# Kernel tuning notes

Measured on AMD Instinct MI355X. Metric: run time of the kernel, lower is better.

The kernel has to match this reference:

```python
import jax, jax.numpy as jnp
import numpy as np

L = 5        # num_layers
D = 128      # emb_dim
H = 2 * D    # mlp hidden
N_ATOM_FEATS, ATOM_VOCAB = 9, 120
N_BOND_FEATS, BOND_VOCAB = 3, 6
BN_EPS = 1e-5


def setup_inputs() -> dict:
    key = jax.random.key(0)
    ks = jax.random.split(key, 16)
    N, E = 200000, 400000
    x = jax.random.randint(ks[0], (N, N_ATOM_FEATS), 0, ATOM_VOCAB)
    edge_index = jax.random.randint(ks[1], (2, E), 0, N)
    edge_attr = jax.random.randint(ks[2], (E, N_BOND_FEATS), 0, BOND_VOCAB)
    s = 0.02
    return {
        "x": x,
        "edge_index": edge_index,
        "edge_attr": edge_attr,
        "atom_emb": jax.random.normal(ks[3], (N_ATOM_FEATS, ATOM_VOCAB, D), jnp.float32) * s,
        "bond_emb": jax.random.normal(ks[4], (L, N_BOND_FEATS, BOND_VOCAB, D), jnp.float32) * s,
        "W1": jax.random.normal(ks[5], (L, D, H), jnp.float32) * s,
        "b1": jnp.zeros((L, H), jnp.float32),
        "bn1_g": jnp.ones((L, H), jnp.float32),
        "bn1_b": jnp.zeros((L, H), jnp.float32),
        "W2": jax.random.normal(ks[6], (L, H, D), jnp.float32) * s,
        "b2": jnp.zeros((L, D), jnp.float32),
        "eps": jnp.zeros((L,), jnp.float32),
        "out_bn_g": jnp.ones((L, D), jnp.float32),
        "out_bn_b": jnp.zeros((L, D), jnp.float32),
    }


def _batchnorm(z, g, b):
    mu = jnp.mean(z, axis=0, keepdims=True)
    var = jnp.var(z, axis=0, keepdims=True)
    return (z - mu) * jax.lax.rsqrt(var + BN_EPS) * g + b


def _multi_embed(tables, idx):
    # tables: [F, V, D], idx: [N, F] -> sum_f tables[f][idx[:, f]] : [N, D]
    gathered = jax.vmap(lambda tab, i: tab[i], in_axes=(0, 1))(tables, idx)  # [F, N, D]
    return jnp.sum(gathered, axis=0)


def reference(x, edge_index, edge_attr, atom_emb, bond_emb, W1, b1, bn1_g, bn1_b,
              W2, b2, eps, out_bn_g, out_bn_b):
    N = x.shape[0]
    src, dst = edge_index[0], edge_index[1]
    h = _multi_embed(atom_emb, x)  # AtomEncoder: [N, D]
    for l in range(L):
        e = _multi_embed(bond_emb[l], edge_attr)          # BondEncoder: [E, D]
        msg = jax.nn.relu(h[src] + e)                     # message
        aggr = jax.ops.segment_sum(msg, dst, num_segments=N)  # scatter-add
        z = (1.0 + eps[l]) * h + aggr                     # GIN combine
        z = jax.nn.relu(_batchnorm(z @ W1[l] + b1[l], bn1_g[l], bn1_b[l]))
        z = z @ W2[l] + b2[l]
        h = jax.nn.relu(_batchnorm(z, out_bn_g[l], out_bn_b[l]))  # relu+dropout(p=0)
    return h  # JK='last'
```

## Files before the change

### kernel.cpp

```cpp
#include <hip/hip_runtime.h>

#define NF_ATOM 9
#define NF_BOND 3
#define DD 128
#define HH 256
#define NLAYER 5
#define NSHARD 32
#define NCODE 216

typedef float fv4 __attribute__((ext_vector_type(4)));
typedef __bf16 bfv8 __attribute__((ext_vector_type(8)));
typedef unsigned int uv4 __attribute__((ext_vector_type(4)));

__device__ inline unsigned short f2bf(float f) {
    unsigned int u = __builtin_bit_cast(unsigned int, f);
    u = u + 0x7FFFu + ((u >> 16) & 1u);
    return (unsigned short)(u >> 16);
}
__device__ inline float bf2f(unsigned short s) {
    unsigned int u = ((unsigned int)s) << 16;
    return __builtin_bit_cast(float, u);
}

__global__ __launch_bounds__(256) void k_atom(const int* __restrict__ x,
        const float* __restrict__ emb, unsigned short* __restrict__ h, int N) {
    int gid = blockIdx.x * 256 + threadIdx.x;
    int n = gid >> 5;
    if (n >= N) return;
    int c = (gid & 31) << 2;
    const int* xr = x + n * NF_ATOM;
    float4 acc = make_float4(0.f, 0.f, 0.f, 0.f);
#pragma unroll
    for (int f = 0; f < NF_ATOM; ++f) {
        int idx = xr[f];
        float4 v = *(const float4*)(emb + ((size_t)(f * 120 + idx) * DD) + c);
        acc.x += v.x; acc.y += v.y; acc.z += v.z; acc.w += v.w;
    }
    ushort4 o;
    o.x = f2bf(acc.x); o.y = f2bf(acc.y); o.z = f2bf(acc.z); o.w = f2bf(acc.w);
    *(ushort4*)(h + (size_t)n * DD + c) = o;
}

__global__ __launch_bounds__(256) void k_wconv(const float* __restrict__ W1,
        const float* __restrict__ W2, unsigned short* __restrict__ W1t,
        unsigned short* __restrict__ W2t) {
    int id = blockIdx.x * 256 + threadIdx.x;
    const int T1 = NLAYER * 4 * 256 * 32;
    if (id < T1) {
        int k = id & 31, n = (id >> 5) & 255, kc = (id >> 13) & 3, l = id >> 15;
        W1t[id] = f2bf(W1[((size_t)(l * 128 + kc * 32 + k)) * 256 + n]);
    } else {
        int id2 = id - T1;
        if (id2 >= NLAYER * 8 * 128 * 32) return;
        int k = id2 & 31, n = (id2 >> 5) & 127, kc = (id2 >> 12) & 7, l = id2 >> 15;
        W2t[id2] = f2bf(W2[((size_t)(l * 256 + kc * 32 + k)) * 128 + n]);
    }
}

__global__ __launch_bounds__(256) void k_bsumtab(const float* __restrict__ bemb,
        float* __restrict__ tab) {
    int id = blockIdx.x * 256 + threadIdx.x;
    if (id >= NLAYER * NCODE * DD) return;
    int c = id & 127;
    int code = (id >> 7) % NCODE;
    int l = id / (NCODE * DD);
    int a0 = code % 6, a1 = (code / 6) % 6, a2 = code / 36;
    const float* bl = bemb + (size_t)l * NF_BOND * 6 * DD;
    tab[id] = bl[(0 * 6 + a0) * DD + c] + bl[(1 * 6 + a1) * DD + c] + bl[(2 * 6 + a2) * DD + c];
}

__global__ __launch_bounds__(256) void k_deg(const int* __restrict__ ei, int* __restrict__ deg, int E) {
    int e = blockIdx.x * 256 + threadIdx.x;
    if (e < E) atomicAdd(&deg[ei[E + e]], 1);
}
__global__ __launch_bounds__(256) void k_bsum(const int* __restrict__ deg, int* __restrict__ bsum, int N) {
    __shared__ int red[256];
    int t = threadIdx.x, b = blockIdx.x;
    int i0 = b * 1024 + t * 4;
    int s = 0;
#pragma unroll
    for (int j = 0; j < 4; ++j) if (i0 + j < N) s += deg[i0 + j];
    red[t] = s; __syncthreads();
    for (int off = 128; off > 0; off >>= 1) {
        if (t < off) red[t] += red[t + off];
        __syncthreads();
    }
    if (t == 0) bsum[b] = red[0];
}
__global__ __launch_bounds__(256) void k_bscan(const int* __restrict__ bsum, int* __restrict__ boff, int nb) {
    __shared__ int ts[256];
    int t = threadIdx.x;
    int v = (t < nb) ? bsum[t] : 0;
    ts[t] = v; __syncthreads();
    for (int off = 1; off < 256; off <<= 1) {
        int u = (t >= off) ? ts[t - off] : 0;
        __syncthreads();
        ts[t] += u;
        __syncthreads();
    }
    if (t < nb) boff[t] = ts[t] - v;
}
__global__ __launch_bounds__(256) void k_csr(const int* deg, const int* __restrict__ boff,
        int* rs, int N, int E) {
    __shared__ int ts[256];
    int t = threadIdx.x, b = blockIdx.x;
    int i0 = b * 1024 + t * 4;
    int d[4];
#pragma unroll
    for (int j = 0; j < 4; ++j) d[j] = (i0 + j < N) ? deg[i0 + j] : 0;
    int tsum = d[0] + d[1] + d[2] + d[3];
    ts[t] = tsum; __syncthreads();
    for (int off = 1; off < 256; off <<= 1) {
        int u = (t >= off) ? ts[t - off] : 0;
        __syncthreads();
        ts[t] += u;
        __syncthreads();
    }
    int base = boff[b] + ts[t] - tsum;
    int p = 0;
#pragma unroll
    for (int j = 0; j < 4; ++j) {
        int dj = d[j];
        if (i0 + j < N) rs[i0 + j] = base + p;
        p += dj;
    }
    if (b == 0 && t == 0) rs[N] = E;
}
__global__ __launch_bounds__(256) void k_scatter(const int* __restrict__ ei,
        const int* __restrict__ ea, int* __restrict__ rs, int* __restrict__ epack, int E) {
    int e = blockIdx.x * 256 + threadIdx.x;
    if (e < E) {
        int pos = atomicAdd(&rs[ei[E + e]], 1);
        int code = ea[e * 3 + 0] + 6 * ea[e * 3 + 1] + 36 * ea[e * 3 + 2];
        epack[pos] = ei[e] | (code << 18);
    }
}

__global__ void k_red(const float* __restrict__ sh, int C, const float* __restrict__ bng,
        const float* __restrict__ bnb, const float* __restrict__ gbias, int useb,
        float invN, float* __restrict__ sc_out, float* __restrict__ sh_out) {
    int t = threadIdx.x;
    if (t >= C) return;
    float a = 0.f, qq = 0.f;
#pragma unroll
    for (int s = 0; s < NSHARD; ++s) {
        a += sh[s * 2 * C + t];
        qq += sh[s * 2 * C + C + t];
    }
    float mu = a * invN;
    float var = qq * invN - mu * mu;
    float r = rsqrtf(var + 1e-5f);
    float sc = bng[t] * r;
    float shift = bnb[t] - mu * sc;
    if (useb) shift += gbias[t] * sc;
    sc_out[t] = sc; sh_out[t] = shift;
}

__device__ inline void edge_acc(ushort4 hv, float4 bv, float4 sc, float4 sh, int mode, float* ag) {
    float h0 = bf2f(hv.x), h1 = bf2f(hv.y), h2 = bf2f(hv.z), h3 = bf2f(hv.w);
    if (mode) {
        h0 = fmaxf(h0 * sc.x + sh.x, 0.f); h1 = fmaxf(h1 * sc.y + sh.y, 0.f);
        h2 = fmaxf(h2 * sc.z + sh.z, 0.f); h3 = fmaxf(h3 * sc.w + sh.w, 0.f);
    }
    ag[0] += fmaxf(h0 + bv.x, 0.f); ag[1] += fmaxf(h1 + bv.y, 0.f);
    ag[2] += fmaxf(h2 + bv.z, 0.f); ag[3] += fmaxf(h3 + bv.w, 0.f);
}

__global__ __launch_bounds__(256) void k_zbuild(const unsigned short* __restrict__ y2h,
        const int* __restrict__ rs, const int* __restrict__ epack,
        const float* __restrict__ btab, const float* __restrict__ sctab,
        const float* __restrict__ shtab, const float* __restrict__ epsv,
        int l, int mode, unsigned short* __restrict__ z, int N) {
    int gid = blockIdx.x * 256 + threadIdx.x;
    int n = gid >> 5;
    if (n >= N) return;
    int c = (gid & 31) << 2;
    float4 sc4 = make_float4(1.f, 1.f, 1.f, 1.f), sh4 = make_float4(0.f, 0.f, 0.f, 0.f);
    if (mode) { sc4 = *(const float4*)(sctab + c); sh4 = *(const float4*)(shtab + c); }
    int p0 = (n == 0) ? 0 : rs[n - 1];
    int p1 = rs[n];
    float ag[4] = {0.f, 0.f, 0.f, 0.f};
    int p = p0;
    for (; p + 2 <= p1; p += 2) {
        int rec0 = epack[p], rec1 = epack[p + 1];
        int s0 = rec0 & 0x3FFFF, s1 = rec1 & 0x3FFFF;
        int c0 = ((unsigned int)rec0) >> 18, c1 = ((unsigned int)rec1) >> 18;
        ushort4 h0 = *(const ushort4*)(y2h + (size_t)s0 * DD + c);
        ushort4 h1 = *(const ushort4*)(y2h + (size_t)s1 * DD + c);
        float4 b0 = *(const float4*)(btab + (size_t)c0 * DD + c);
        float4 b1 = *(const float4*)(btab + (size_t)c1 * DD + c);
        edge_acc(h0, b0, sc4, sh4, mode, ag);
        edge_acc(h1, b1, sc4, sh4, mode, ag);
    }
    if (p < p1) {
        int rec = epack[p];
        int s0 = rec & 0x3FFFF;
        int c0 = ((unsigned int)rec) >> 18;
        ushort4 h0 = *(const ushort4*)(y2h + (size_t)s0 * DD + c);
        float4 b0 = *(const float4*)(btab + (size_t)c0 * DD + c);
        edge_acc(h0, b0, sc4, sh4, mode, ag);
    }
    float ep = 1.0f + epsv[l];
    ushort4 sv = *(const ushort4*)(y2h + (size_t)n * DD + c);
    float hz[4] = {bf2f(sv.x), bf2f(sv.y), bf2f(sv.z), bf2f(sv.w)};
    if (mode) {
        hz[0] = fmaxf(hz[0] * sc4.x + sh4.x, 0.f);
        hz[1] = fmaxf(hz[1] * sc4.y + sh4.y, 0.f);
        hz[2] = fmaxf(hz[2] * sc4.z + sh4.z, 0.f);
        hz[3] = fmaxf(hz[3] * sc4.w + sh4.w, 0.f);
    }
    ushort4 o;
    o.x = f2bf(ep * hz[0] + ag[0]);
    o.y = f2bf(ep * hz[1] + ag[1]);
    o.z = f2bf(ep * hz[2] + ag[2]);
    o.w = f2bf(ep * hz[3] + ag[3]);
    *(ushort4*)(z + (size_t)n * DD + c) = o;
}

__global__ __launch_bounds__(256) void k_stat1(const unsigned short* __restrict__ z,
        const unsigned short* __restrict__ W1l, const float* __restrict__ bias,
        float* __restrict__ shard, int N) {
    __shared__ uv4 zt[64 * 16];
    __shared__ uv4 wt[256 * 4];
    int tid = threadIdx.x;
    int row0 = blockIdx.x * 64;
    int wave = tid >> 6, lane = tid & 63, lq = lane >> 4, lr = lane & 15;
    int rbase = tid >> 4, gz = tid & 15;

    uv4 zr[4];
#pragma unroll
    for (int i = 0; i < 4; ++i)
        zr[i] = *(const uv4*)(z + (size_t)(row0 + i * 16 + rbase) * DD + gz * 8);
    const uv4* wsrc = (const uv4*)W1l;
    uv4 wr[4];
#pragma unroll
    for (int i = 0; i < 4; ++i) wr[i] = wsrc[i * 256 + tid];
#pragma unroll
    for (int i = 0; i < 4; ++i) {
        int row = i * 16 + rbase;
        zt[row * 16 + (gz ^ (row & 15))] = zr[i];
    }

    fv4 acc[4][4];
#pragma unroll
    for (int m = 0; m < 4; ++m)
#pragma unroll
        for (int nb = 0; nb < 4; ++nb) acc[m][nb] = (fv4){0.f, 0.f, 0.f, 0.f};

    for (int kc = 0; kc < 4; ++kc) {
        __syncthreads();
#pragma unroll
        for (int i = 0; i < 4; ++i) {
            int g = i * 256 + tid;
            int wn = g >> 2, gw = g & 3;
            wt[wn * 4 + (gw ^ ((wn >> 1) & 3))] = wr[i];
        }
        __syncthreads();
        if (kc < 3) {
#pragma unroll
            for (int i = 0; i < 4; ++i) wr[i] = wsrc[(size_t)(kc + 1) * 1024 + i * 256 + tid];
        }
        bfv8 a[4], b[4];
#pragma unroll
        for (int m = 0; m < 4; ++m) {
            int row = m * 16 + lr;
            a[m] = __builtin_bit_cast(bfv8, zt[row * 16 + ((kc * 4 + lq) ^ (row & 15))]);
        }
#pragma unroll
        for (int nb = 0; nb < 4; ++nb) {
            int col = wave * 64 + nb * 16 + lr;
            b[nb] = __builtin_bit_cast(bfv8, wt[col * 4 + (lq ^ ((col >> 1) & 3))]);
        }
#pragma unroll
        for (int m = 0; m < 4; ++m)
#pragma unroll
            for (int nb = 0; nb < 4; ++nb)
                acc[m][nb] = __builtin_amdgcn_mfma_f32_16x16x32_bf16(a[m], b[nb], acc[m][nb], 0, 0, 0);
    }

    float bv[4], s[4], q[4];
#pragma unroll
    for (int nb = 0; nb < 4; ++nb) {
        bv[nb] = bias[wave * 64 + nb * 16 + lr];
        s[nb] = 0.f; q[nb] = 0.f;
    }
#pragma unroll
    for (int m = 0; m < 4; ++m)
#pragma unroll
        for (int nb = 0; nb < 4; ++nb)
#pragma unroll
            for (int r = 0; r < 4; ++r) {
                float v = acc[m][nb][r] + bv[nb];
                s[nb] += v; q[nb] += v * v;
            }
#pragma unroll
    for (int nb = 0; nb < 4; ++nb) {
        s[nb] += __shfl_xor(s[nb], 16); s[nb] += __shfl_xor(s[nb], 32);
        q[nb] += __shfl_xor(q[nb], 16); q[nb] += __shfl_xor(q[nb], 32);
    }
    if (lane < 16) {
        int shb = (blockIdx.x & (NSHARD - 1)) * 512;
#pragma unroll
        for (int nb = 0; nb < 4; ++nb) {
            int col = wave * 64 + nb * 16 + lr;
            atomicAdd(shard + shb + col, s[nb]);
            atomicAdd(shard + shb + 256 + col, q[nb]);
        }
    }
}

__global__ __launch_bounds__(256) void k_fgemm(const unsigned short* __restrict__ z,
        const unsigned short* __restrict__ W1l, const unsigned short* __restrict__ W2l,
        const float* __restrict__ sc1, const float* __restrict__ sh1,
        const float* __restrict__ bias2,
        unsigned short* __restrict__ y2h, float* __restrict__ shard, int N) {
    __shared__ uv4 smem[2560];
    uv4* zt = smem;
    uv4* wt = smem + 1024;
    uv4* at = smem;
    uv4* wt2 = smem + 2048;
    int tid = threadIdx.x;
    int row0 = blockIdx.x * 64;
    int wave = tid >> 6, lane = tid & 63, lq = lane >> 4, lr = lane & 15;
    int rbase = tid >> 4, gz = tid & 15;

    uv4 zr[4];
#pragma unroll
    for (int i = 0; i < 4; ++i)
        zr[i] = *(const uv4*)(z + (size_t)(row0 + i * 16 + rbase) * DD + gz * 8);
    const uv4* w1src = (const uv4*)W1l;
    uv4 wr[4];
#pragma unroll
    for (int i = 0; i < 4; ++i) wr[i] = w1src[i * 256 + tid];
#pragma unroll
    for (int i = 0; i < 4; ++i) {
        int row = i * 16 + rbase;
        zt[row * 16 + (gz ^ (row & 15))] = zr[i];
    }

    fv4 acc1[4][4];
#pragma unroll
    for (int mc = 0; mc < 4; ++mc)
#pragma unroll
        for (int nr = 0; nr < 4; ++nr) acc1[mc][nr] = (fv4){0.f, 0.f, 0.f, 0.f};

    for (int kc = 0; kc < 4; ++kc) {
        __syncthreads();
#pragma unroll
        for (int i = 0; i < 4; ++i) {
            int g = i * 256 + tid;
            int wn = g >> 2, gw = g & 3;
            wt[wn * 4 + (gw ^ ((wn >> 1) & 3))] = wr[i];
        }
        __syncthreads();
        if (kc < 3) {
#pragma unroll
            for (int i = 0; i < 4; ++i) wr[i] = w1src[(size_t)(kc + 1) * 1024 + i * 256 + tid];
        }
        bfv8 wf[4], zf[4];
#pragma unroll
        for (int mc = 0; mc < 4; ++mc) {
            int col = wave * 64 + mc * 16 + lr;
            wf[mc] = __builtin_bit_cast(bfv8, wt[col * 4 + (lq ^ ((col >> 1) & 3))]);
        }
#pragma unroll
        for (int nr = 0; nr < 4; ++nr) {
            int row = nr * 16 + lr;
            zf[nr] = __builtin_bit_cast(bfv8, zt[row * 16 + ((kc * 4 + lq) ^ (row & 15))]);
        }
#pragma unroll
        for (int mc = 0; mc < 4; ++mc)
#pragma unroll
            for (int nr = 0; nr < 4; ++nr)
                acc1[mc][nr] = __builtin_amdgcn_mfma_f32_16x16x32_bf16(wf[mc], zf[nr], acc1[mc][nr], 0, 0, 0);
    }
    __syncthreads();

    const uv4* w2src = (const uv4*)W2l;
    uv4 wr2[2];
    wr2[0] = w2src[tid]; wr2[1] = w2src[256 + tid];

#pragma unroll
    for (int mc = 0; mc < 4; ++mc) {
        int ycol0 = wave * 64 + mc * 16 + lq * 4;
        float4 s4 = *(const float4*)(sc1 + ycol0);
        float4 h4 = *(const float4*)(sh1 + ycol0);
        int gg = wave * 8 + mc * 2 + (lq >> 1);
#pragma unroll
        for (int nr = 0; nr < 4; ++nr) {
            int zrow = nr * 16 + lr;
            float v0 = fmaxf(acc1[mc][nr][0] * s4.x + h4.x, 0.f);
            float v1 = fmaxf(acc1[mc][nr][1] * s4.y + h4.y, 0.f);
            float v2 = fmaxf(acc1[mc][nr][2] * s4.z + h4.z, 0.f);
            float v3 = fmaxf(acc1[mc][nr][3] * s4.w + h4.w, 0.f);
            uint2 pk;
            pk.x = (unsigned int)f2bf(v0) | ((unsigned int)f2bf(v1) << 16);
            pk.y = (unsigned int)f2bf(v2) | ((unsigned int)f2bf(v3) << 16);
            int gs = gg ^ (zrow & 15);
            ((uint2*)at)[(zrow * 32 + gs) * 2 + (lq & 1)] = pk;
        }
    }

    fv4 acc2[4][2];
#pragma unroll
    for (int m = 0; m < 4; ++m) { acc2[m][0] = (fv4){0.f,0.f,0.f,0.f}; acc2[m][1] = (fv4){0.f,0.f,0.f,0.f}; }

    for (int kc = 0; kc < 8; ++kc) {
        __syncthreads();
        {
            int wn = tid >> 2, gw = tid & 3;
            wt2[wn * 4 + (gw ^ ((wn >> 1) & 3))] = wr2[0];
            int g3 = 256 + tid, wn3 = g3 >> 2, gw3 = g3 & 3;
            wt2[wn3 * 4 + (gw3 ^ ((wn3 >> 1) & 3))] = wr2[1];
        }
        __syncthreads();
        if (kc < 7) {
            wr2[0] = w2src[(size_t)(kc + 1) * 512 + tid];
            wr2[1] = w2src[(size_t)(kc + 1) * 512 + 256 + tid];
        }
        bfv8 a[4], b[2];
#pragma unroll
        for (int m = 0; m < 4; ++m) {
            int row = m * 16 + lr;
            a[m] = __builtin_bit_cast(bfv8, at[row * 32 + ((kc * 4 + lq) ^ (row & 15))]);
        }
#pragma unroll
        for (int nb = 0; nb < 2; ++nb) {
            int col = wave * 32 + nb * 16 + lr;
            b[nb] = __builtin_bit_cast(bfv8, wt2[col * 4 + (lq ^ ((col >> 1) & 3))]);
        }
#pragma unroll
        for (int m = 0; m < 4; ++m)
#pragma unroll
            for (int nb = 0; nb < 2; ++nb)
                acc2[m][nb] = __builtin_amdgcn_mfma_f32_16x16x32_bf16(a[m], b[nb], acc2[m][nb], 0, 0, 0);
    }

    float bv[2], s[2], q[2];
#pragma unroll
    for (int nb = 0; nb < 2; ++nb) {
        bv[nb] = bias2[wave * 32 + nb * 16 + lr];
        s[nb] = 0.f; q[nb] = 0.f;
    }
#pragma unroll
    for (int m = 0; m < 4; ++m)
#pragma unroll
        for (int nb = 0; nb < 2; ++nb) {
            int col = wave * 32 + nb * 16 + lr;
#pragma unroll
            for (int r = 0; r < 4; ++r) {
                float v = acc2[m][nb][r] + bv[nb];
                unsigned short ub = f2bf(v);
                float vr = bf2f(ub);
                int row = row0 + m * 16 + lq * 4 + r;
                y2h[(size_t)row * DD + col] = ub;
                s[nb] += vr; q[nb] += vr * vr;
            }
        }
#pragma unroll
    for (int nb = 0; nb < 2; ++nb) {
        s[nb] += __shfl_xor(s[nb], 16); s[nb] += __shfl_xor(s[nb], 32);
        q[nb] += __shfl_xor(q[nb], 16); q[nb] += __shfl_xor(q[nb], 32);
    }
    if (lane < 16) {
        int shb = (blockIdx.x & (NSHARD - 1)) * 256;
#pragma unroll
        for (int nb = 0; nb < 2; ++nb) {
            int col = wave * 32 + nb * 16 + lr;
            atomicAdd(shard + shb + col, s[nb]);
            atomicAdd(shard + shb + 128 + col, q[nb]);
        }
    }
}

__global__ __launch_bounds__(256) void k_bnfinal(const unsigned short* __restrict__ y2h,
        const float* __restrict__ sc2, const float* __restrict__ sh2,
        float* __restrict__ out, int N) {
    size_t base = ((size_t)blockIdx.x * 256 + threadIdx.x) * 4;
    if (base >= (size_t)N * DD) return;
    int c = (int)(base & (DD - 1));
    ushort4 v = *(const ushort4*)(y2h + base);
    float4 s = *(const float4*)(sc2 + c);
    float4 t = *(const float4*)(sh2 + c);
    float4 o;
    o.x = fmaxf(bf2f(v.x) * s.x + t.x, 0.f);
    o.y = fmaxf(bf2f(v.y) * s.y + t.y, 0.f);
    o.z = fmaxf(bf2f(v.z) * s.z + t.z, 0.f);
    o.w = fmaxf(bf2f(v.w) * s.w + t.w, 0.f);
    *(float4*)(out + base) = o;
}

extern "C" void kernel_launch(void* const* d_in, const int* in_sizes, int n_in,
                              void* d_out, int out_size, void* d_ws, size_t ws_size,
                              hipStream_t stream) {
    const int* x = (const int*)d_in[0];
    const int* ei = (const int*)d_in[1];
    const int* ea = (const int*)d_in[2];
    const float* atom_emb = (const float*)d_in[3];
    const float* bond_emb = (const float*)d_in[4];
    const float* W1 = (const float*)d_in[5];
    const float* b1 = (const float*)d_in[6];
    const float* bn1_g = (const float*)d_in[7];
    const float* bn1_b = (const float*)d_in[8];
    const float* W2 = (const float*)d_in[9];
    const float* b2 = (const float*)d_in[10];
    const float* epsv = (const float*)d_in[11];
    const float* obn_g = (const float*)d_in[12];
    const float* obn_b = (const float*)d_in[13];
    int N = in_sizes[0] / NF_ATOM;
    int E = in_sizes[1] / 2;

    char* wsb = (char*)d_ws;
    unsigned short* y2h = (unsigned short*)wsb;
    unsigned short* zb = (unsigned short*)(wsb + (size_t)N * 256);
    int* epack = (int*)(wsb + (size_t)N * 512);
    unsigned short* w1t = (unsigned short*)(wsb + (size_t)N * 512 + (size_t)E * 4);
    unsigned short* w2t = w1t + 163840;
    float* btab = (float*)((char*)w2t + 327680);
    float* sc1 = btab + NLAYER * NCODE * DD;
    float* sh1 = sc1 + 256;
    float* sc2 = sh1 + 256;
    float* sh2 = sc2 + 128;
    float* shard1 = sh2 + 128;
    float* shard2 = shard1 + NSHARD * 512;
    int* rsarr = (int*)(shard2 + NSHARD * 256);
    int* bsum = rsarr + (N + 1);
    int* boff = bsum + 256;
    float invN = 1.0f / (float)N;
    int nbk = (N + 1023) / 1024;

    k_wconv<<<1280, 256, 0, stream>>>(W1, W2, w1t, w2t);
    k_bsumtab<<<(NLAYER * NCODE * DD + 255) / 256, 256, 0, stream>>>(bond_emb, btab);
    hipMemsetAsync(rsarr, 0, ((size_t)N + 1) * 4, stream);
    k_deg<<<(E + 255) / 256, 256, 0, stream>>>(ei, rsarr, E);
    k_bsum<<<nbk, 256, 0, stream>>>(rsarr, bsum, N);
    k_bscan<<<1, 256, 0, stream>>>(bsum, boff, nbk);
    k_csr<<<nbk, 256, 0, stream>>>(rsarr, boff, rsarr, N, E);
    k_scatter<<<(E + 255) / 256, 256, 0, stream>>>(ei, ea, rsarr, epack, E);
    k_atom<<<(N * 32 + 255) / 256, 256, 0, stream>>>(x, atom_emb, y2h, N);

    int gb = N / 64;
    for (int l = 0; l < NLAYER; ++l) {
        hipMemsetAsync(shard1, 0, (size_t)NSHARD * 768 * sizeof(float), stream);
        k_zbuild<<<(N * 32 + 255) / 256, 256, 0, stream>>>(y2h, rsarr, epack,
                btab + (size_t)l * NCODE * DD, sc2, sh2, epsv, l, (l == 0) ? 0 : 1, zb, N);
        k_stat1<<<gb, 256, 0, stream>>>(zb, w1t + (size_t)l * 32768, b1 + l * HH, shard1, N);
        k_red<<<1, 256, 0, stream>>>(shard1, 256, bn1_g + l * HH, bn1_b + l * HH,
                b1 + l * HH, 1, invN, sc1, sh1);
        k_fgemm<<<gb, 256, 0, stream>>>(zb, w1t + (size_t)l * 32768, w2t + (size_t)l * 32768,
                sc1, sh1, b2 + l * DD, y2h, shard2, N);
        k_red<<<1, 128, 0, stream>>>(shard2, 128, obn_g + l * DD, obn_b + l * DD,
                (const float*)nullptr, 0, invN, sc2, sh2);
    }
    k_bnfinal<<<(int)(((size_t)N * DD / 4 + 255) / 256), 256, 0, stream>>>(
            y2h, sc2, sh2, (float*)d_out, N);
}
```

Baseline: 791.3 us.

## Split bf16 weights into hi/lo parts for higher-precision GEMMs, hoist shard zeroing

Each weight is stored as a bf16 high part plus a bf16 residual. Every GEMM K-loop is doubled so activations multiply both parts and recover near-fp32 weight precision. The per-layer memset of the statistics shards is replaced by one upfront memset over per-layer shard buffers. This is mainly an accuracy fix that doubles MFMA work and weight traffic in the stat and fused GEMM kernels; the memset hoist only saves a few launches.

Result: slower. 1.007 ms (+27.3%).

```diff
diff --git a/kernel.cpp b/kernel.cpp
--- a/kernel.cpp
+++ b/kernel.cpp
@@ -48,12 +48,20 @@
     const int T1 = NLAYER * 4 * 256 * 32;
     if (id < T1) {
         int k = id & 31, n = (id >> 5) & 255, kc = (id >> 13) & 3, l = id >> 15;
-        W1t[id] = f2bf(W1[((size_t)(l * 128 + kc * 32 + k)) * 256 + n]);
+        int o = id & 32767;
+        float w = W1[((size_t)(l * 128 + kc * 32 + k)) * 256 + n];
+        unsigned short hi = f2bf(w);
+        W1t[(size_t)l * 65536 + o] = hi;
+        W1t[(size_t)l * 65536 + 32768 + o] = f2bf(w - bf2f(hi));
     } else {
         int id2 = id - T1;
         if (id2 >= NLAYER * 8 * 128 * 32) return;
         int k = id2 & 31, n = (id2 >> 5) & 127, kc = (id2 >> 12) & 7, l = id2 >> 15;
-        W2t[id2] = f2bf(W2[((size_t)(l * 256 + kc * 32 + k)) * 128 + n]);
+        int o = id2 & 32767;
+        float w = W2[((size_t)(l * 256 + kc * 32 + k)) * 128 + n];
+        unsigned short hi = f2bf(w);
+        W2t[(size_t)l * 65536 + o] = hi;
+        W2t[(size_t)l * 65536 + 32768 + o] = f2bf(w - bf2f(hi));
     }
 }
 
@@ -247,7 +255,7 @@
 #pragma unroll
         for (int nb = 0; nb < 4; ++nb) acc[m][nb] = (fv4){0.f, 0.f, 0.f, 0.f};
 
-    for (int kc = 0; kc < 4; ++kc) {
+    for (int kc = 0; kc < 8; ++kc) {
         __syncthreads();
 #pragma unroll
         for (int i = 0; i < 4; ++i) {
@@ -256,7 +264,7 @@
             wt[wn * 4 + (gw ^ ((wn >> 1) & 3))] = wr[i];
         }
         __syncthreads();
-        if (kc < 3) {
+        if (kc < 7) {
 #pragma unroll
             for (int i = 0; i < 4; ++i) wr[i] = wsrc[(size_t)(kc + 1) * 1024 + i * 256 + tid];
         }
@@ -264,7 +272,7 @@
 #pragma unroll
         for (int m = 0; m < 4; ++m) {
             int row = m * 16 + lr;
-            a[m] = __builtin_bit_cast(bfv8, zt[row * 16 + ((kc * 4 + lq) ^ (row & 15))]);
+            a[m] = __builtin_bit_cast(bfv8, zt[row * 16 + (((kc & 3) * 4 + lq) ^ (row & 15))]);
         }
 #pragma unroll
         for (int nb = 0; nb < 4; ++nb) {
@@ -344,7 +352,7 @@
 #pragma unroll
         for (int nr = 0; nr < 4; ++nr) acc1[mc][nr] = (fv4){0.f, 0.f, 0.f, 0.f};
 
-    for (int kc = 0; kc < 4; ++kc) {
+    for (int kc = 0; kc < 8; ++kc) {
         __syncthreads();
 #pragma unroll
         for (int i = 0; i < 4; ++i) {
@@ -353,7 +361,7 @@
             wt[wn * 4 + (gw ^ ((wn >> 1) & 3))] = wr[i];
         }
         __syncthreads();
-        if (kc < 3) {
+        if (kc < 7) {
 #pragma unroll
             for (int i = 0; i < 4; ++i) wr[i] = w1src[(size_t)(kc + 1) * 1024 + i * 256 + tid];
         }
@@ -366,7 +374,7 @@
 #pragma unroll
         for (int nr = 0; nr < 4; ++nr) {
             int row = nr * 16 + lr;
-            zf[nr] = __builtin_bit_cast(bfv8, zt[row * 16 + ((kc * 4 + lq) ^ (row & 15))]);
+            zf[nr] = __builtin_bit_cast(bfv8, zt[row * 16 + (((kc & 3) * 4 + lq) ^ (row & 15))]);
         }
 #pragma unroll
         for (int mc = 0; mc < 4; ++mc)
@@ -405,7 +413,7 @@
 #pragma unroll
     for (int m = 0; m < 4; ++m) { acc2[m][0] = (fv4){0.f,0.f,0.f,0.f}; acc2[m][1] = (fv4){0.f,0.f,0.f,0.f}; }
 
-    for (int kc = 0; kc < 8; ++kc) {
+    for (int kc = 0; kc < 16; ++kc) {
         __syncthreads();
         {
             int wn = tid >> 2, gw = tid & 3;
@@ -414,7 +422,7 @@
             wt2[wn3 * 4 + (gw3 ^ ((wn3 >> 1) & 3))] = wr2[1];
         }
         __syncthreads();
-        if (kc < 7) {
+        if (kc < 15) {
             wr2[0] = w2src[(size_t)(kc + 1) * 512 + tid];
             wr2[1] = w2src[(size_t)(kc + 1) * 512 + 256 + tid];
         }
@@ -422,7 +430,7 @@
 #pragma unroll
         for (int m = 0; m < 4; ++m) {
             int row = m * 16 + lr;
-            a[m] = __builtin_bit_cast(bfv8, at[row * 32 + ((kc * 4 + lq) ^ (row & 15))]);
+            a[m] = __builtin_bit_cast(bfv8, at[row * 32 + (((kc & 7) * 4 + lq) ^ (row & 15))]);
         }
 #pragma unroll
         for (int nb = 0; nb < 2; ++nb) {
@@ -515,15 +523,17 @@
     unsigned short* zb = (unsigned short*)(wsb + (size_t)N * 256);
     int* epack = (int*)(wsb + (size_t)N * 512);
     unsigned short* w1t = (unsigned short*)(wsb + (size_t)N * 512 + (size_t)E * 4);
-    unsigned short* w2t = w1t + 163840;
-    float* btab = (float*)((char*)w2t + 327680);
+    unsigned short* w2t = w1t + 327680;
+    float* btab = (float*)((char*)w2t + 655360);
     float* sc1 = btab + NLAYER * NCODE * DD;
     float* sh1 = sc1 + 256;
     float* sc2 = sh1 + 256;
     float* sh2 = sc2 + 128;
-    float* shard1 = sh2 + 128;
-    float* shard2 = shard1 + NSHARD * 512;
-    int* rsarr = (int*)(shard2 + NSHARD * 256);
+    float* shardbase = sh2 + 128;
+    float* shard1 = shardbase;
+    float* shard2 = shard1 + (size_t)NLAYER * NSHARD * 512;
+    size_t zero_f = (size_t)NLAYER * (NSHARD * 512 + NSHARD * 256);
+    int* rsarr = (int*)(shard2 + (size_t)NLAYER * NSHARD * 256);
     int* bsum = rsarr + (N + 1);
     int* boff = bsum + 256;
     float invN = 1.0f / (float)N;
@@ -532,6 +542,7 @@
     k_wconv<<<1280, 256, 0, stream>>>(W1, W2, w1t, w2t);
     k_bsumtab<<<(NLAYER * NCODE * DD + 255) / 256, 256, 0, stream>>>(bond_emb, btab);
     hipMemsetAsync(rsarr, 0, ((size_t)N + 1) * 4, stream);
+    hipMemsetAsync(shardbase, 0, zero_f * sizeof(float), stream);
     k_deg<<<(E + 255) / 256, 256, 0, stream>>>(ei, rsarr, E);
     k_bsum<<<nbk, 256, 0, stream>>>(rsarr, bsum, N);
     k_bscan<<<1, 256, 0, stream>>>(bsum, boff, nbk);
@@ -541,15 +552,16 @@
 
     int gb = N / 64;
     for (int l = 0; l < NLAYER; ++l) {
-        hipMemsetAsync(shard1, 0, (size_t)NSHARD * 768 * sizeof(float), stream);
+        float* sh1d = shard1 + (size_t)l * NSHARD * 512;
+        float* sh2d = shard2 + (size_t)l * NSHARD * 256;
         k_zbuild<<<(N * 32 + 255) / 256, 256, 0, stream>>>(y2h, rsarr, epack,
                 btab + (size_t)l * NCODE * DD, sc2, sh2, epsv, l, (l == 0) ? 0 : 1, zb, N);
-        k_stat1<<<gb, 256, 0, stream>>>(zb, w1t + (size_t)l * 32768, b1 + l * HH, shard1, N);
-        k_red<<<1, 256, 0, stream>>>(shard1, 256, bn1_g + l * HH, bn1_b + l * HH,
+        k_stat1<<<gb, 256, 0, stream>>>(zb, w1t + (size_t)l * 65536, b1 + l * HH, sh1d, N);
+        k_red<<<1, 256, 0, stream>>>(sh1d, 256, bn1_g + l * HH, bn1_b + l * HH,
                 b1 + l * HH, 1, invN, sc1, sh1);
-        k_fgemm<<<gb, 256, 0, stream>>>(zb, w1t + (size_t)l * 32768, w2t + (size_t)l * 32768,
-                sc1, sh1, b2 + l * DD, y2h, shard2, N);
-        k_red<<<1, 128, 0, stream>>>(shard2, 128, obn_g + l * DD, obn_b + l * DD,
+        k_fgemm<<<gb, 256, 0, stream>>>(zb, w1t + (size_t)l * 65536, w2t + (size_t)l * 65536,
+                sc1, sh1, b2 + l * DD, y2h, sh2d, N);
+        k_red<<<1, 128, 0, stream>>>(sh2d, 128, obn_g + l * DD, obn_b + l * DD,
                 (const float*)nullptr, 0, invN, sc2, sh2);
     }
     k_bnfinal<<<(int)(((size_t)N * DD / 4 + 255) / 256), 256, 0, stream>>>(
```
